# Kernel tuning notes

Hardware: AMD Instinct MI355X
Metric: run time of the kernel (lower is better)

The kernel has to match this reference:

```python
import jax, jax.numpy as jnp
import numpy as np

COLOR_SIZE = 8
FILTERS = 64
LAYERS = 4
CUMSUM_NORM = 256 * 256 * 3  # hardcoded in original: /256/256/3


def setup_inputs() -> dict:
    key = jax.random.key(0)
    k0, k1, k2, k3 = jax.random.split(key, 4)
    s = 0.05
    example = jax.random.randint(k0, (4, 256, 256, 3), 0, COLOR_SIZE, dtype=jnp.int32)
    # per-channel Dense stacks: layer 0 has input dim 1, layers 1..3 have input dim FILTERS
    W_in_first = jax.random.normal(k1, (3, 1, FILTERS), dtype=jnp.float32) * s
    b_in_first = jnp.zeros((3, FILTERS), dtype=jnp.float32)
    W_in_rest = jax.random.normal(k2, (LAYERS - 1, 3, FILTERS, FILTERS), dtype=jnp.float32) * s
    b_in_rest = jnp.zeros((LAYERS - 1, 3, FILTERS), dtype=jnp.float32)
    W_final = jax.random.normal(k3, (3, FILTERS, COLOR_SIZE), dtype=jnp.float32) * s
    b_final = jnp.zeros((3, COLOR_SIZE), dtype=jnp.float32)
    return {
        "example": example,
        "W_in_first": W_in_first, "b_in_first": b_in_first,
        "W_in_rest": W_in_rest, "b_in_rest": b_in_rest,
        "W_final": W_final, "b_final": b_final,
    }


def reference(example, W_in_first, b_in_first, W_in_rest, b_in_rest, W_final, b_final):
    # example: [B, H, W, 3] int in [0, COLOR_SIZE)
    x = example.astype(jnp.float32) / COLOR_SIZE * 2.0 - 1.0
    B, H, W, _ = x.shape
    L = H * W
    x = x.reshape(B, L, 3, 1)

    def layer(x, Wl, bl):
        # per-channel dense + relu: [B, L, 3, din] x [3, din, dout] -> [B, L, 3, dout]
        x = jax.nn.relu(jnp.einsum('blcd,cde->blce', x, Wl) + bl)
        # flatten channels into the sequence and take causal running sum
        x = x.reshape(B, L * 3, FILTERS)
        x = jnp.cumsum(x, axis=-2) / CUMSUM_NORM
        return x.reshape(B, L, 3, FILTERS)

    x = layer(x, W_in_first, b_in_first)
    for i in range(LAYERS - 1):
        x = layer(x, W_in_rest[i], b_in_rest[i])

    # final per-channel dense to color logits (no activation)
    x = jnp.einsum('blcd,cde->blce', x, W_final) + b_final
    return x.reshape(B, H, W, 3, COLOR_SIZE)
```

## Files before the change

### kernel.cpp

```cpp
#include <hip/hip_runtime.h>
#include <stdint.h>


#define BB 4
#define SP 65536
#define SS 196608
#define CI 1024
#define NG 16
#define INVN (1.0f / 196608.0f)

typedef __attribute__((ext_vector_type(8))) _Float16 half8;
typedef __attribute__((ext_vector_type(4))) float    f32x4;

#define WAVE_FENCE() do {                                    \
    __builtin_amdgcn_sched_barrier(0);                       \
    asm volatile("s_waitcnt lgkmcnt(0)" ::: "memory");       \
    __builtin_amdgcn_sched_barrier(0);                       \
} while (0)

__global__ __launch_bounds__(256)
void prep(const int* __restrict__ ex, const float* __restrict__ W0,
          const float* __restrict__ b0, const float* __restrict__ Wr,
          const float* __restrict__ Wfin,
          _Float16* __restrict__ Wt16, float* __restrict__ Wd32T,
          _Float16* __restrict__ Wf16p,
          float* __restrict__ Wf32, float* __restrict__ tab32,
          int* __restrict__ Hsub, int* __restrict__ Hgrp)
{
    __shared__ int hist[16][24];
    int tid = threadIdx.x, bi = blockIdx.x;
    int b = bi >> 6, g = (bi >> 2) & 15, q = bi & 3;
    for (int i = tid; i < 384; i += 256) hist[i / 24][i % 24] = 0;
    __syncthreads();
    for (int it = 0; it < 4; ++it) {
        int pl = it * 256 + tid;
        const int* ep = ex + ((size_t)b * SP + g * 4096 + q * 1024 + pl) * 3;
        int j = pl >> 6;
        atomicAdd(&hist[j][ep[0]], 1);
        atomicAdd(&hist[j][8 + ep[1]], 1);
        atomicAdd(&hist[j][16 + ep[2]], 1);
    }
    __syncthreads();
    for (int i = tid; i < 384; i += 256) {
        int j = i / 24, cv = i % 24;
        Hsub[(size_t)(b * CI + g * 64 + q * 16 + j) * 24 + cv] = hist[j][cv];
    }
    if (tid < 24) {
        int s = 0;
        for (int j = 0; j < 16; ++j) s += hist[j][tid];
        atomicAdd(&Hgrp[(size_t)(b * NG + g) * 24 + tid], s);
    }
    {
        int i0 = bi * 256 + tid, nth = 256 * 256;
        for (int idx = i0; idx < 36864; idx += nth) {
            int d = idx & 63, f = (idx >> 6) & 63, lc = idx >> 12;
            float v = Wr[(size_t)(lc * 64 + d) * 64 + f];
            Wt16[idx]  = (_Float16)v;
            Wd32T[idx] = v;
        }
        for (int idx = i0; idx < 3072; idx += nth) {
            int d = idx & 63, n = (idx >> 6) & 15, c = idx >> 10;
            Wf16p[idx] = (n < 8) ? (_Float16)Wfin[(size_t)(c * 64 + d) * 8 + n]
                                 : (_Float16)0.f;
        }
        for (int idx = i0; idx < 1536; idx += nth) {
            int d = idx & 63, ck = idx >> 6;
            Wf32[idx] = Wfin[(size_t)((ck >> 3) * 64 + d) * 8 + (ck & 7)];
        }
        for (int idx = i0; idx < 1536; idx += nth) {
            int f = idx & 63, v = (idx >> 6) & 7, c = idx >> 9;
            float xv = v * 0.25f - 1.0f;
            tab32[idx] = fmaxf(W0[c * 64 + f] * xv + b0[c * 64 + f], 0.f);
        }
    }
}

__global__ __launch_bounds__(256, 4)
void midA(const int* __restrict__ ex,
          const int* __restrict__ Hsub, const int* __restrict__ Hgrp,
          const float* __restrict__ tab32,
          const _Float16* __restrict__ W16, const float* __restrict__ WT32,
          const float* __restrict__ bias, _Float16* __restrict__ Y,
          float* __restrict__ A64, float* __restrict__ Ggrp)
{
    __shared__ float stab[1536];
    __shared__ __align__(16) _Float16 bounce3[3][64 * 72];
    __shared__ float segwt[3][4][64];
    __shared__ float basearr[192];
    __shared__ float hpart[4][24];
    __shared__ float carry[64];

    int tid = threadIdx.x, bi = blockIdx.x;
    int b = bi >> 10, ci = bi & 1023, g = ci >> 6, cr = ci & 63;
    int w = tid >> 6, ln = tid & 63, lm = ln & 15, lq = ln >> 4;
    int P0 = ci * 64;

    for (int i = tid; i < 1536; i += 256) stab[i] = tab32[i];
    if (ln < 24) {
        float s = 0.f;
        for (int j = w; j < g; j += 4)
            s += (float)Hgrp[(size_t)(b * NG + j) * 24 + ln];
        const int* hp = Hsub + (size_t)(b * CI + g * 64) * 24 + ln;
        for (int j = w; j < cr; j += 4) s += (float)hp[j * 24];
        hpart[w][ln] = s;
    }
    __syncthreads();

    float y0[3][16];
    {
#pragma unroll
        for (int p = 0; p < 16; ++p) {
            const int* ep = ex + ((size_t)b * SP + P0 + w * 16 + p) * 3;
            y0[0][p] = stab[ep[0] * 64 + ln];
            y0[1][p] = stab[(8 + ep[1]) * 64 + ln];
            y0[2][p] = stab[(16 + ep[2]) * 64 + ln];
        }
#pragma unroll
        for (int c = 0; c < 3; ++c)
#pragma unroll
            for (int p = 1; p < 16; ++p) y0[c][p] += y0[c][p - 1];
#pragma unroll
        for (int c = 0; c < 3; ++c) segwt[c][w][ln] = y0[c][15];
    }
    if (tid < 64) {
        float c0 = 0.f;
#pragma unroll
        for (int cv = 0; cv < 24; ++cv) {
            float cnt = hpart[0][cv] + hpart[1][cv] + hpart[2][cv] + hpart[3][cv];
            c0 += cnt * stab[cv * 64 + tid];
        }
        carry[tid] = c0;
    }
    __syncthreads();

    {
        float off0[3];
#pragma unroll
        for (int c = 0; c < 3; ++c) {
            float o = 0.f;
            for (int w2 = 0; w2 < w; ++w2) o += segwt[c][w2][ln];
            off0[c] = o;
        }
#pragma unroll
        for (int p = 0; p < 16; ++p) {
            float S0 = y0[0][p] + off0[0], S1 = y0[1][p] + off0[1], S2 = y0[2][p] + off0[2];
            float P1 = p ? y0[1][p - 1] + off0[1] : off0[1];
            float P2 = p ? y0[2][p - 1] + off0[2] : off0[2];
            int row = w * 16 + p;
            bounce3[0][row * 72 + ln] = (_Float16)(S0 + P1 + P2);
            bounce3[1][row * 72 + ln] = (_Float16)(S0 + S1 + P2);
            bounce3[2][row * 72 + ln] = (_Float16)(S0 + S1 + S2);
        }
    }
    if (tid < 192) {
        int c = tid >> 6, f = tid & 63;
        const float* wp = WT32 + (size_t)(c * 64 + f) * 64;
        float a = 0.f;
#pragma unroll 16
        for (int d = 0; d < 64; ++d) a += carry[d] * wp[d];
        basearr[tid] = bias[tid] + INVN * a;
    }
    __syncthreads();

    f32x4 acc[3][4];
#pragma unroll
    for (int c = 0; c < 3; ++c) {
        const half8* bb = (const half8*)&bounce3[c][0];
        half8 a0 = bb[(w * 16 + lm) * 9 + lq];
        half8 a1 = bb[(w * 16 + lm) * 9 + 4 + lq];
#pragma unroll
        for (int nt = 0; nt < 4; ++nt) {
            const half8* bp = (const half8*)(W16 + (size_t)(c * 64 + nt * 16 + lm) * 64);
            f32x4 t = {0.f, 0.f, 0.f, 0.f};
            t = __builtin_amdgcn_mfma_f32_16x16x32_f16(a0, bp[lq],     t, 0, 0, 0);
            t = __builtin_amdgcn_mfma_f32_16x16x32_f16(a1, bp[4 + lq], t, 0, 0, 0);
            acc[c][nt] = t;
        }
    }

    float s[3][4][4], wexcl[3][4];
#pragma unroll
    for (int c = 0; c < 3; ++c)
#pragma unroll
        for (int nt = 0; nt < 4; ++nt) {
            float base = basearr[c * 64 + nt * 16 + lm];
            float run = 0.f;
#pragma unroll
            for (int r = 0; r < 4; ++r) {
                float yv = fmaxf(base + INVN * acc[c][nt][r], 0.f);
                run += yv; s[c][nt][r] = run;
            }
            float v = run;
            float t1 = __shfl_up(v, 16); if (lq >= 1) v += t1;
            float t2 = __shfl_up(v, 32); if (lq >= 2) v += t2;
            wexcl[c][nt] = v - run;
            if (lq == 3) segwt[c][w][nt * 16 + lm] = v;
        }
    __syncthreads();

    {
        float off[3][4], tot[3][4];
#pragma unroll
        for (int c = 0; c < 3; ++c)
#pragma unroll
            for (int nt = 0; nt < 4; ++nt) {
                float o = wexcl[c][nt], ts = 0.f;
#pragma unroll
                for (int w2 = 0; w2 < 4; ++w2) {
                    float wv = segwt[c][w2][nt * 16 + lm];
                    ts += wv;
                    if (w2 < w) o += wv;
                }
                off[c][nt] = o; tot[c][nt] = ts;
            }
        if (w == 0 && lq == 0)
#pragma unroll
            for (int nt = 0; nt < 4; ++nt) {
                float t3 = tot[0][nt] + tot[1][nt] + tot[2][nt];
                A64[(size_t)(b * CI + ci) * 64 + nt * 16 + lm] = t3;
                atomicAdd(&Ggrp[(size_t)(b * NG + g) * 64 + nt * 16 + lm], t3);
            }
#pragma unroll
        for (int nt = 0; nt < 4; ++nt)
#pragma unroll
            for (int r = 0; r < 4; ++r) {
                float S0 = off[0][nt] + s[0][nt][r];
                float S1 = off[1][nt] + s[1][nt][r];
                float S2 = off[2][nt] + s[2][nt][r];
                float P1 = off[1][nt] + (r ? s[1][nt][r - 1] : 0.f);
                float P2 = off[2][nt] + (r ? s[2][nt][r - 1] : 0.f);
                int row = w * 16 + lq * 4 + r;
                bounce3[0][row * 72 + nt * 16 + lm] = (_Float16)(S0 + P1 + P2);
                bounce3[1][row * 72 + nt * 16 + lm] = (_Float16)(S0 + S1 + P2);
                bounce3[2][row * 72 + nt * 16 + lm] = (_Float16)(S0 + S1 + S2);
            }
    }
    __syncthreads();
#pragma unroll
    for (int q = 0; q < 6; ++q) {
        int idx = q * 256 + tid;
        int c = idx >> 9, rem = idx & 511;
        int pix = rem >> 3, f8 = rem & 7;
        half8 v = *(const half8*)&bounce3[c][pix * 72 + f8 * 8];
        ((half8*)(Y + ((size_t)(b * 3 + c) * SP + P0 + pix) * 64))[f8] = v;
    }
}

__global__ __launch_bounds__(256, 4)
void midB(const _Float16* __restrict__ Yin, _Float16* __restrict__ Yout,
          const float* __restrict__ A64p, const float* __restrict__ Ggrp_p,
          const _Float16* __restrict__ W16, const float* __restrict__ WT32,
          const float* __restrict__ bias,
          float* __restrict__ A64, float* __restrict__ Ggrp)
{
    __shared__ float cpart[4][64];
    __shared__ float carry4[4][64];
    __shared__ float basearr4[4][192];
    __shared__ __align__(16) _Float16 wb[4][16 * 72];

    int tid = threadIdx.x, bi = blockIdx.x;
    int b = bi >> 8, cb = bi & 255;
    int ci0 = cb * 4, g = cb >> 4, cr0 = ci0 & 63;
    int w = tid >> 6, ln = tid & 63, lm = ln & 15, lq = ln >> 4;
    int ci = ci0 + w;
    int P0 = ci * 64;

    {
        float s = 0.f;
        for (int j = w; j < g; j += 4)
            s += Ggrp_p[(size_t)(b * NG + j) * 64 + ln];
        const float* ap = A64p + (size_t)(b * CI + g * 64) * 64 + ln;
        for (int j = w; j < cr0; j += 4) s += ap[j * 64];
        cpart[w][ln] = s;
    }
    __syncthreads();
    {
        float cw = cpart[0][ln] + cpart[1][ln] + cpart[2][ln] + cpart[3][ln];
        const float* ap = A64p + (size_t)(b * CI + ci0) * 64 + ln;
        for (int t = 0; t < w; ++t) cw += ap[t * 64];
        carry4[w][ln] = cw;
    }
    __syncthreads();
    if (tid < 192) {
        int c = tid >> 6, f = tid & 63;
        const float* wp = WT32 + (size_t)(c * 64 + f) * 64;
        float a0 = 0.f, a1 = 0.f, a2 = 0.f, a3 = 0.f;
#pragma unroll 8
        for (int d = 0; d < 64; ++d) {
            float wv = wp[d];
            a0 += carry4[0][d] * wv; a1 += carry4[1][d] * wv;
            a2 += carry4[2][d] * wv; a3 += carry4[3][d] * wv;
        }
        float bz = bias[tid];
        basearr4[0][tid] = bz + INVN * a0;
        basearr4[1][tid] = bz + INVN * a1;
        basearr4[2][tid] = bz + INVN * a2;
        basearr4[3][tid] = bz + INVN * a3;
    }
    __syncthreads();

    float bse[3][4];
#pragma unroll
    for (int c = 0; c < 3; ++c)
#pragma unroll
        for (int nt = 0; nt < 4; ++nt)
            bse[c][nt] = basearr4[w][c * 64 + nt * 16 + lm];
    float roff[3][4] = {{0.f,0.f,0.f,0.f},{0.f,0.f,0.f,0.f},{0.f,0.f,0.f,0.f}};
    _Float16* wbw = &wb[w][0];

#pragma unroll
    for (int pq = 0; pq < 4; ++pq) {
        half8 af0[3], af1[3];
#pragma unroll
        for (int c = 0; c < 3; ++c) {
            const half8* ap = (const half8*)(Yin +
                ((size_t)(b * 3 + c) * SP + P0 + pq * 16 + lm) * 64);
            af0[c] = ap[lq]; af1[c] = ap[4 + lq];
        }
        f32x4 acc[3][4];
#pragma unroll
        for (int c = 0; c < 3; ++c)
#pragma unroll
            for (int nt = 0; nt < 4; ++nt) {
                const half8* bp = (const half8*)(W16 + (size_t)(c * 64 + nt * 16 + lm) * 64);
                f32x4 t = {0.f, 0.f, 0.f, 0.f};
                t = __builtin_amdgcn_mfma_f32_16x16x32_f16(af0[c], bp[lq],     t, 0, 0, 0);
                t = __builtin_amdgcn_mfma_f32_16x16x32_f16(af1[c], bp[4 + lq], t, 0, 0, 0);
                acc[c][nt] = t;
            }

        float s[3][4][4], off[3][4];
#pragma unroll
        for (int c = 0; c < 3; ++c)
#pragma unroll
            for (int nt = 0; nt < 4; ++nt) {
                float base = bse[c][nt];
                float run = 0.f;
#pragma unroll
                for (int r = 0; r < 4; ++r) {
                    float yv = fmaxf(base + INVN * acc[c][nt][r], 0.f);
                    run += yv; s[c][nt][r] = run;
                }
                float v = run;
                float t1 = __shfl_up(v, 16); if (lq >= 1) v += t1;
                float t2 = __shfl_up(v, 32); if (lq >= 2) v += t2;
                off[c][nt] = roff[c][nt] + (v - run);
                roff[c][nt] += __shfl(v, 48 + lm);
            }

#pragma unroll
        for (int c = 0; c < 3; ++c) {
#pragma unroll
            for (int nt = 0; nt < 4; ++nt) {
                float offT = off[0][nt] + off[1][nt] + off[2][nt];
#pragma unroll
                for (int r = 0; r < 4; ++r) {
                    float s1p = r ? s[1][nt][r - 1] : 0.f;
                    float s2p = r ? s[2][nt][r - 1] : 0.f;
                    float V = offT + s[0][nt][r];
                    float ov = (c == 0) ? (V + s1p + s2p)
                             : (c == 1) ? (V + s[1][nt][r] + s2p)
                                        : (V + s[1][nt][r] + s[2][nt][r]);
                    wbw[(lq * 4 + r) * 72 + nt * 16 + lm] = (_Float16)ov;
                }
            }
            WAVE_FENCE();
            const half8* bb = (const half8*)wbw;
            _Float16* Yc = Yout + ((size_t)(b * 3 + c) * SP + P0 + pq * 16) * 64;
#pragma unroll
            for (int q = 0; q < 2; ++q) {
                int idx = q * 64 + ln, pix = idx >> 3, f8 = idx & 7;
                ((half8*)(Yc + (size_t)pix * 64))[f8] = bb[pix * 9 + f8];
            }
        }
    }

    if (lq == 0)
#pragma unroll
        for (int nt = 0; nt < 4; ++nt) {
            float t3 = roff[0][nt] + roff[1][nt] + roff[2][nt];
            A64[(size_t)(b * CI + ci) * 64 + nt * 16 + lm] = t3;
            atomicAdd(&Ggrp[(size_t)(b * NG + g) * 64 + nt * 16 + lm], t3);
        }
}

__global__ __launch_bounds__(256, 4)
void midC(const _Float16* __restrict__ Yin,
          const float* __restrict__ A64p, const float* __restrict__ Ggrp_p,
          const _Float16* __restrict__ W16, const float* __restrict__ WT32,
          const float* __restrict__ bias,
          const _Float16* __restrict__ Wf16p, const float* __restrict__ bfin,
          float* __restrict__ out, float* __restrict__ A64, float* __restrict__ Ggrp)
{
    __shared__ float cpart[4][64];
    __shared__ float carry4[4][64];
    __shared__ float basearr4[4][192];
    __shared__ __align__(16) _Float16 wb[4][16 * 72];

    int tid = threadIdx.x, bi = blockIdx.x;
    int b = bi >> 8, cb = bi & 255;
    int ci0 = cb * 4, g = cb >> 4, cr0 = ci0 & 63;
    int w = tid >> 6, ln = tid & 63, lm = ln & 15, lq = ln >> 4;
    int ci = ci0 + w;
    int P0 = ci * 64;

    {
        float s = 0.f;
        for (int j = w; j < g; j += 4)
            s += Ggrp_p[(size_t)(b * NG + j) * 64 + ln];
        const float* ap = A64p + (size_t)(b * CI + g * 64) * 64 + ln;
        for (int j = w; j < cr0; j += 4) s += ap[j * 64];
        cpart[w][ln] = s;
    }
    __syncthreads();
    {
        float cw = cpart[0][ln] + cpart[1][ln] + cpart[2][ln] + cpart[3][ln];
        const float* ap = A64p + (size_t)(b * CI + ci0) * 64 + ln;
        for (int t = 0; t < w; ++t) cw += ap[t * 64];
        carry4[w][ln] = cw;
    }
    __syncthreads();
    if (tid < 192) {
        int c = tid >> 6, f = tid & 63;
        const float* wp = WT32 + (size_t)(c * 64 + f) * 64;
        float a0 = 0.f, a1 = 0.f, a2 = 0.f, a3 = 0.f;
#pragma unroll 8
        for (int d = 0; d < 64; ++d) {
            float wv = wp[d];
            a0 += carry4[0][d] * wv; a1 += carry4[1][d] * wv;
            a2 += carry4[2][d] * wv; a3 += carry4[3][d] * wv;
        }
        float bz = bias[tid];
        basearr4[0][tid] = bz + INVN * a0;
        basearr4[1][tid] = bz + INVN * a1;
        basearr4[2][tid] = bz + INVN * a2;
        basearr4[3][tid] = bz + INVN * a3;
    }
    __syncthreads();

    float bse[3][4];
#pragma unroll
    for (int c = 0; c < 3; ++c)
#pragma unroll
        for (int nt = 0; nt < 4; ++nt)
            bse[c][nt] = basearr4[w][c * 64 + nt * 16 + lm];
    float roff[3][4] = {{0.f,0.f,0.f,0.f},{0.f,0.f,0.f,0.f},{0.f,0.f,0.f,0.f}};
    _Float16* wbw = &wb[w][0];

#pragma unroll
    for (int pq = 0; pq < 4; ++pq) {
        half8 af0[3], af1[3];
#pragma unroll
        for (int c = 0; c < 3; ++c) {
            const half8* ap = (const half8*)(Yin +
                ((size_t)(b * 3 + c) * SP + P0 + pq * 16 + lm) * 64);
            af0[c] = ap[lq]; af1[c] = ap[4 + lq];
        }
        f32x4 acc[3][4];
#pragma unroll
        for (int c = 0; c < 3; ++c)
#pragma unroll
            for (int nt = 0; nt < 4; ++nt) {
                const half8* bp = (const half8*)(W16 + (size_t)(c * 64 + nt * 16 + lm) * 64);
                f32x4 t = {0.f, 0.f, 0.f, 0.f};
                t = __builtin_amdgcn_mfma_f32_16x16x32_f16(af0[c], bp[lq],     t, 0, 0, 0);
                t = __builtin_amdgcn_mfma_f32_16x16x32_f16(af1[c], bp[4 + lq], t, 0, 0, 0);
                acc[c][nt] = t;
            }

        float s[3][4][4], off[3][4];
#pragma unroll
        for (int c = 0; c < 3; ++c)
#pragma unroll
            for (int nt = 0; nt < 4; ++nt) {
                float base = bse[c][nt];
                float run = 0.f;
#pragma unroll
                for (int r = 0; r < 4; ++r) {
                    float yv = fmaxf(base + INVN * acc[c][nt][r], 0.f);
                    run += yv; s[c][nt][r] = run;
                }
                float v = run;
                float t1 = __shfl_up(v, 16); if (lq >= 1) v += t1;
                float t2 = __shfl_up(v, 32); if (lq >= 2) v += t2;
                off[c][nt] = roff[c][nt] + (v - run);
                roff[c][nt] += __shfl(v, 48 + lm);
            }

#pragma unroll
        for (int c = 0; c < 3; ++c) {
#pragma unroll
            for (int nt = 0; nt < 4; ++nt) {
                float offT = off[0][nt] + off[1][nt] + off[2][nt];
#pragma unroll
                for (int r = 0; r < 4; ++r) {
                    float s1p = r ? s[1][nt][r - 1] : 0.f;
                    float s2p = r ? s[2][nt][r - 1] : 0.f;
                    float V = offT + s[0][nt][r];
                    float ov = (c == 0) ? (V + s1p + s2p)
                             : (c == 1) ? (V + s[1][nt][r] + s2p)
                                        : (V + s[1][nt][r] + s[2][nt][r]);
                    wbw[(lq * 4 + r) * 72 + nt * 16 + lm] = (_Float16)ov;
                }
            }
            WAVE_FENCE();
            const half8* bb = (const half8*)wbw;
            half8 fa0 = bb[lm * 9 + lq];
            half8 fa1 = bb[lm * 9 + 4 + lq];
            const half8* fb = (const half8*)(Wf16p + (size_t)(c * 16 + lm) * 64);
            f32x4 t = {0.f, 0.f, 0.f, 0.f};
            t = __builtin_amdgcn_mfma_f32_16x16x32_f16(fa0, fb[lq],     t, 0, 0, 0);
            t = __builtin_amdgcn_mfma_f32_16x16x32_f16(fa1, fb[4 + lq], t, 0, 0, 0);
            if (lm < 8) {
                float bz = bfin[c * 8 + lm];
                float* ob = out + ((size_t)b * SS +
                    (size_t)(P0 + pq * 16 + lq * 4) * 3 + c) * 8 + lm;
#pragma unroll
                for (int r = 0; r < 4; ++r)
                    ob[r * 24] = bz + INVN * t[r];
            }
            WAVE_FENCE();
        }
    }

    if (lq == 0)
#pragma unroll
        for (int nt = 0; nt < 4; ++nt) {
            float t3 = roff[0][nt] + roff[1][nt] + roff[2][nt];
            A64[(size_t)(b * CI + ci) * 64 + nt * 16 + lm] = t3;
            atomicAdd(&Ggrp[(size_t)(b * NG + g) * 64 + nt * 16 + lm], t3);
        }
}

__global__ __launch_bounds__(256, 4)
void fixk(const float* __restrict__ A64p, const float* __restrict__ Ggrp_p,
          const float* __restrict__ Wf32, float* __restrict__ out)
{
    __shared__ float cpart[4][64];
    __shared__ float carry[64];
    __shared__ float part[24][8];
    __shared__ float vfix[24];
    int tid = threadIdx.x, bi = blockIdx.x;
    int b = bi >> 10, ci = bi & 1023, g = ci >> 6, cr = ci & 63;
    int w = tid >> 6, ln = tid & 63;
    int P0 = ci * 64;

    {
        float s = 0.f;
        for (int j = w; j < g; j += 4)
            s += Ggrp_p[(size_t)(b * NG + j) * 64 + ln];
        const float* ap = A64p + (size_t)(b * CI + g * 64) * 64 + ln;
        for (int j = w; j < cr; j += 4) s += ap[j * 64];
        cpart[w][ln] = s;
    }
    __syncthreads();
    if (tid < 64)
        carry[tid] = cpart[0][tid] + cpart[1][tid] + cpart[2][tid] + cpart[3][tid];
    __syncthreads();
    if (tid < 192) {
        int ck = tid >> 3, sg = tid & 7;
        const float* wp = Wf32 + ck * 64 + sg * 8;
        const float* cp = carry + sg * 8;
        float vf = 0.f;
#pragma unroll
        for (int d = 0; d < 8; ++d) vf += cp[d] * wp[d];
        part[ck][sg] = vf;
    }
    __syncthreads();
    if (tid < 24) {
        float vf = 0.f;
#pragma unroll
        for (int j = 0; j < 8; ++j) vf += part[tid][j];
        vfix[tid] = INVN * vf;
    }
    __syncthreads();
    float4* obase = (float4*)(out + ((size_t)b * SS + (size_t)P0 * 3) * 8);
#pragma unroll
    for (int k = 0; k < 2; ++k) {
        int idx = k * 256 + tid;
        if (idx < 384) {
            int sub = (idx % 6) * 4;
            float4 v = obase[idx];
            v.x += vfix[sub];
            v.y += vfix[sub + 1];
            v.z += vfix[sub + 2];
            v.w += vfix[sub + 3];
            obase[idx] = v;
        }
    }
}

extern "C" void kernel_launch(void* const* d_in, const int* in_sizes, int n_in,
                              void* d_out, int out_size, void* d_ws, size_t ws_size,
                              hipStream_t stream)
{
    const int*   ex   = (const int*)d_in[0];
    const float* W0   = (const float*)d_in[1];
    const float* b0   = (const float*)d_in[2];
    const float* Wr   = (const float*)d_in[3];
    const float* br   = (const float*)d_in[4];
    const float* Wfin = (const float*)d_in[5];
    const float* bfin = (const float*)d_in[6];
    float* out = (float*)d_out;

    char* ws = (char*)d_ws;
    size_t off = 0;
    _Float16* Y = (_Float16*)(ws + off); off += (size_t)BB * 3 * SP * 64 * 2;
    float* Ggrp1 = (float*)(ws + off); off += (size_t)BB * NG * 64 * 4;
    float* Ggrp2 = (float*)(ws + off); off += (size_t)BB * NG * 64 * 4;
    float* Ggrp3 = (float*)(ws + off); off += (size_t)BB * NG * 64 * 4;
    float* A64_1 = (float*)(ws + off); off += (size_t)BB * CI * 64 * 4;
    float* A64_2 = (float*)(ws + off); off += (size_t)BB * CI * 64 * 4;
    float* A64_3 = (float*)(ws + off); off += (size_t)BB * CI * 64 * 4;
    int* Hsub = (int*)(ws + off); off += (size_t)BB * CI * 24 * 4;
    int* Hgrp = (int*)(ws + off); off += (size_t)BB * NG * 24 * 4;
    _Float16* Wt16  = (_Float16*)(ws + off); off += 36864 * 2;
    float* Wd32T = (float*)(ws + off); off += 36864 * 4;
    _Float16* Wf16p = (_Float16*)(ws + off); off += 3072 * 2;
    float* Wf32  = (float*)(ws + off); off += 1536 * 4;
    float* tab32 = (float*)(ws + off); off += 1536 * 4;

    hipMemsetAsync(Ggrp1, 0, 3 * (size_t)BB * NG * 64 * 4, stream);
    hipMemsetAsync(Hgrp, 0, (size_t)BB * NG * 24 * 4, stream);
    prep<<<256, 256, 0, stream>>>(ex, W0, b0, Wr, Wfin,
                                  Wt16, Wd32T, Wf16p, Wf32, tab32, Hsub, Hgrp);
    midA<<<4096, 256, 0, stream>>>(ex, Hsub, Hgrp, tab32,
                                   Wt16, Wd32T, br, Y, A64_1, Ggrp1);
    midB<<<1024, 256, 0, stream>>>(Y, Y, A64_1, Ggrp1,
                                   Wt16 + 12288, Wd32T + 12288, br + 192,
                                   A64_2, Ggrp2);
    midC<<<1024, 256, 0, stream>>>(Y, A64_2, Ggrp2,
                                   Wt16 + 24576, Wd32T + 24576, br + 384,
                                   Wf16p, bfin, out, A64_3, Ggrp3);
    fixk<<<4096, 256, 0, stream>>>(A64_3, Ggrp3, Wf32, out);
}
```

Before: 374.8 us.

## Drop memsets, remove wave fences, stage final output stores through LDS

Two hipMemsetAsync calls are replaced: the Ggrp zeroing moves into the prep kernel, and the Hgrp atomics become per-quarter histogram writes that midA sums itself. The explicit lgkmcnt wave fences around the per-wave LDS bounce buffers are removed, which relies on the compiler inserting the needed waits. midC now stages the strided logits writes in shared memory and emits coalesced float4 stores. midA reads the original Wr layout with strided access instead of the transposed copy. Together these aim to cut launch overhead and uncoalesced stores, at the cost of some extra LDS use and a possible LDS ordering risk.

```diff
diff --git a/kernel.cpp b/kernel.cpp
--- a/kernel.cpp
+++ b/kernel.cpp
@@ -11,12 +11,6 @@
 
 typedef __attribute__((ext_vector_type(8))) _Float16 half8;
 typedef __attribute__((ext_vector_type(4))) float    f32x4;
-
-#define WAVE_FENCE() do {                                    \
-    __builtin_amdgcn_sched_barrier(0);                       \
-    asm volatile("s_waitcnt lgkmcnt(0)" ::: "memory");       \
-    __builtin_amdgcn_sched_barrier(0);                       \
-} while (0)
 
 __global__ __launch_bounds__(256)
 void prep(const int* __restrict__ ex, const float* __restrict__ W0,
@@ -25,7 +19,8 @@
           _Float16* __restrict__ Wt16, float* __restrict__ Wd32T,
           _Float16* __restrict__ Wf16p,
           float* __restrict__ Wf32, float* __restrict__ tab32,
-          int* __restrict__ Hsub, int* __restrict__ Hgrp)
+          int* __restrict__ Hsub, int* __restrict__ Hqrt,
+          float* __restrict__ Gz)
 {
     __shared__ int hist[16][24];
     int tid = threadIdx.x, bi = blockIdx.x;
@@ -48,10 +43,12 @@
     if (tid < 24) {
         int s = 0;
         for (int j = 0; j < 16; ++j) s += hist[j][tid];
-        atomicAdd(&Hgrp[(size_t)(b * NG + g) * 24 + tid], s);
+        Hqrt[((size_t)(b * NG + g) * 4 + q) * 24 + tid] = s;
     }
     {
         int i0 = bi * 256 + tid, nth = 256 * 256;
+        for (int idx = i0; idx < 12288; idx += nth)
+            Gz[idx] = 0.f;
         for (int idx = i0; idx < 36864; idx += nth) {
             int d = idx & 63, f = (idx >> 6) & 63, lc = idx >> 12;
             float v = Wr[(size_t)(lc * 64 + d) * 64 + f];
@@ -77,9 +74,9 @@
 
 __global__ __launch_bounds__(256, 4)
 void midA(const int* __restrict__ ex,
-          const int* __restrict__ Hsub, const int* __restrict__ Hgrp,
+          const int* __restrict__ Hsub, const int* __restrict__ Hqrt,
           const float* __restrict__ tab32,
-          const _Float16* __restrict__ W16, const float* __restrict__ WT32,
+          const _Float16* __restrict__ W16, const float* __restrict__ Wd32,
           const float* __restrict__ bias, _Float16* __restrict__ Y,
           float* __restrict__ A64, float* __restrict__ Ggrp)
 {
@@ -98,8 +95,10 @@
     for (int i = tid; i < 1536; i += 256) stab[i] = tab32[i];
     if (ln < 24) {
         float s = 0.f;
-        for (int j = w; j < g; j += 4)
-            s += (float)Hgrp[(size_t)(b * NG + j) * 24 + ln];
+        for (int j = w; j < g; j += 4) {
+            const int* hq = Hqrt + ((size_t)(b * NG + j) * 4) * 24 + ln;
+            s += (float)(hq[0] + hq[24] + hq[48] + hq[72]);
+        }
         const int* hp = Hsub + (size_t)(b * CI + g * 64) * 24 + ln;
         for (int j = w; j < cr; j += 4) s += (float)hp[j * 24];
         hpart[w][ln] = s;
@@ -154,10 +153,9 @@
     }
     if (tid < 192) {
         int c = tid >> 6, f = tid & 63;
-        const float* wp = WT32 + (size_t)(c * 64 + f) * 64;
+        const float* wp = Wd32 + (size_t)(c * 64) * 64 + f;
         float a = 0.f;
-#pragma unroll 16
-        for (int d = 0; d < 64; ++d) a += carry[d] * wp[d];
+        for (int d = 0; d < 64; ++d) a += carry[d] * wp[d * 64];
         basearr[tid] = bias[tid] + INVN * a;
     }
     __syncthreads();
@@ -364,7 +362,6 @@
                     wbw[(lq * 4 + r) * 72 + nt * 16 + lm] = (_Float16)ov;
                 }
             }
-            WAVE_FENCE();
             const half8* bb = (const half8*)wbw;
             _Float16* Yc = Yout + ((size_t)(b * 3 + c) * SP + P0 + pq * 16) * 64;
 #pragma unroll
@@ -396,6 +393,7 @@
     __shared__ float carry4[4][64];
     __shared__ float basearr4[4][192];
     __shared__ __align__(16) _Float16 wb[4][16 * 72];
+    __shared__ __align__(16) float outst[4][16 * 28];
 
     int tid = threadIdx.x, bi = blockIdx.x;
     int b = bi >> 8, cb = bi & 255;
@@ -446,6 +444,7 @@
             bse[c][nt] = basearr4[w][c * 64 + nt * 16 + lm];
     float roff[3][4] = {{0.f,0.f,0.f,0.f},{0.f,0.f,0.f,0.f},{0.f,0.f,0.f,0.f}};
     _Float16* wbw = &wb[w][0];
+    float* outw = &outst[w][0];
 
 #pragma unroll
     for (int pq = 0; pq < 4; ++pq) {
@@ -503,7 +502,6 @@
                     wbw[(lq * 4 + r) * 72 + nt * 16 + lm] = (_Float16)ov;
                 }
             }
-            WAVE_FENCE();
             const half8* bb = (const half8*)wbw;
             half8 fa0 = bb[lm * 9 + lq];
             half8 fa1 = bb[lm * 9 + 4 + lq];
@@ -513,13 +511,22 @@
             t = __builtin_amdgcn_mfma_f32_16x16x32_f16(fa1, fb[4 + lq], t, 0, 0, 0);
             if (lm < 8) {
                 float bz = bfin[c * 8 + lm];
-                float* ob = out + ((size_t)b * SS +
-                    (size_t)(P0 + pq * 16 + lq * 4) * 3 + c) * 8 + lm;
 #pragma unroll
                 for (int r = 0; r < 4; ++r)
-                    ob[r * 24] = bz + INVN * t[r];
-            }
-            WAVE_FENCE();
+                    outw[(lq * 4 + r) * 28 + c * 8 + lm] = bz + INVN * t[r];
+            }
+        }
+        {
+            float4* obq = (float4*)(out + ((size_t)b * SS +
+                                           (size_t)(P0 + pq * 16) * 3) * 8);
+#pragma unroll
+            for (int k = 0; k < 2; ++k) {
+                int idx = k * 64 + ln;
+                if (idx < 96) {
+                    int pix = idx / 6, sub = (idx % 6) * 4;
+                    obq[idx] = *(const float4*)&outw[pix * 28 + sub];
+                }
+            }
         }
     }
 
@@ -613,19 +620,18 @@
     float* A64_2 = (float*)(ws + off); off += (size_t)BB * CI * 64 * 4;
     float* A64_3 = (float*)(ws + off); off += (size_t)BB * CI * 64 * 4;
     int* Hsub = (int*)(ws + off); off += (size_t)BB * CI * 24 * 4;
-    int* Hgrp = (int*)(ws + off); off += (size_t)BB * NG * 24 * 4;
+    int* Hqrt = (int*)(ws + off); off += (size_t)BB * NG * 4 * 24 * 4;
     _Float16* Wt16  = (_Float16*)(ws + off); off += 36864 * 2;
     float* Wd32T = (float*)(ws + off); off += 36864 * 4;
     _Float16* Wf16p = (_Float16*)(ws + off); off += 3072 * 2;
     float* Wf32  = (float*)(ws + off); off += 1536 * 4;
     float* tab32 = (float*)(ws + off); off += 1536 * 4;
 
-    hipMemsetAsync(Ggrp1, 0, 3 * (size_t)BB * NG * 64 * 4, stream);
-    hipMemsetAsync(Hgrp, 0, (size_t)BB * NG * 24 * 4, stream);
     prep<<<256, 256, 0, stream>>>(ex, W0, b0, Wr, Wfin,
-                                  Wt16, Wd32T, Wf16p, Wf32, tab32, Hsub, Hgrp);
-    midA<<<4096, 256, 0, stream>>>(ex, Hsub, Hgrp, tab32,
-                                   Wt16, Wd32T, br, Y, A64_1, Ggrp1);
+                                  Wt16, Wd32T, Wf16p, Wf32, tab32,
+                                  Hsub, Hqrt, Ggrp1);
+    midA<<<4096, 256, 0, stream>>>(ex, Hsub, Hqrt, tab32,
+                                   Wt16, Wr, br, Y, A64_1, Ggrp1);
     midB<<<1024, 256, 0, stream>>>(Y, Y, A64_1, Ggrp1,
                                    Wt16 + 12288, Wd32T + 12288, br + 192,
                                    A64_2, Ggrp2);
```

New measurement: 380.8 us. Within noise of the previous version (+1.6%).
